# Kernel tuning notes

Hardware: AMD Instinct MI355X
Metric: run time of the kernel (lower is better)

## Reference

```python
import jax, jax.numpy as jnp
import numpy as np

N_RULES = 64  # R
OUT_PER_RULE = 64  # O, fc out = R*O = 4096


def setup_inputs() -> dict:
    key = jax.random.key(0)
    k1, k2, k3, k4 = jax.random.split(key, 4)
    S, D_IN = 8192, 1024
    RO = N_RULES * OUT_PER_RULE
    X = jax.random.normal(k1, (S, D_IN), dtype=jnp.float32)
    # torch.nn.Linear-style weight [out, in] and bias [out]
    W = jax.random.normal(k2, (RO, D_IN), dtype=jnp.float32) * (1.0 / np.sqrt(D_IN))
    b = jax.random.normal(k3, (RO,), dtype=jnp.float32) * 0.01
    # rule firing strengths (computed under no_grad in the original)
    lambdas = jax.random.uniform(k4, (S, N_RULES), dtype=jnp.float32)
    return {"X": X, "W": W, "b": b, "lambdas": lambdas}


def reference(X, W, b, lambdas):
    # fc + sigmoid: [S, R*O]
    H = jax.nn.sigmoid(X @ W.T + b)
    S = H.shape[0]
    # apply_rule_strength: block-diagonal lambda_eye @ H^T is exactly a
    # rule-weighted sum over the R consecutive O-sized blocks of H.
    Hr = H.reshape(S, N_RULES, OUT_PER_RULE)  # [S, R, O]
    Y = jnp.einsum("sr,sro->so", lambdas, Hr)  # [S, O]
    return Y
```

## Files before the change

kernel.cpp:

```cpp
#include <hip/hip_runtime.h>

#define S_DIM 8192
#define K_DIM 1024
#define RO_DIM 4096
#define O_DIM 64
#define SO (S_DIM * O_DIM)

typedef __attribute__((ext_vector_type(8))) __bf16 bf16x8;
typedef __attribute__((ext_vector_type(4))) float floatx4;
typedef __attribute__((ext_vector_type(4))) unsigned short ushx4;

__device__ inline unsigned short f2bf(float f) {
  unsigned u = __builtin_bit_cast(unsigned, f);
  u += 0x7fff + ((u >> 16) & 1);
  return (unsigned short)(u >> 16);
}
__device__ inline float bf2f(unsigned short h) {
  unsigned u = ((unsigned)h) << 16;
  return __builtin_bit_cast(float, u);
}

__global__ __launch_bounds__(256) void cast_kernel(const float* __restrict__ X,
                                                   const float* __restrict__ W,
                                                   unsigned short* __restrict__ Xb,
                                                   unsigned short* __restrict__ Wb) {
  const int NX4 = (S_DIM * K_DIM) / 4;
#pragma unroll
  for (int i = 0; i < 4; ++i) {
    int g = blockIdx.x * 1024 + i * 256 + threadIdx.x;
    float4 v;
    unsigned short* dst;
    if (g < NX4) {
      v = ((const float4*)X)[g];
      dst = Xb + (size_t)g * 4;
    } else {
      int j = g - NX4;
      v = ((const float4*)W)[j];
      dst = Wb + (size_t)j * 4;
    }
    ushx4 o;
    o.x = f2bf(v.x); o.y = f2bf(v.y); o.z = f2bf(v.z); o.w = f2bf(v.w);
    *(ushx4*)dst = o;
  }
}

__global__ __launch_bounds__(256) void gemm_kernel(const unsigned short* __restrict__ Xb,
                                                   const unsigned short* __restrict__ Wb,
                                                   const float* __restrict__ bias,
                                                   const float* __restrict__ lam,
                                                   unsigned short* __restrict__ partial) {
  __shared__ __align__(16) unsigned char smem[33792];
  unsigned short* Atile = (unsigned short*)smem;
  unsigned short* Btile = (unsigned short*)(smem + 16384);
  float* lamsh = (float*)(smem + 32768);

  const int t = threadIdx.x;
  const int lane = t & 63;
  const int w = t >> 6;
  const int wm = w & 1;
  const int oh = w >> 1;
  const int quad = lane >> 4;
  const int l16 = lane & 15;
  const int gm0 = blockIdx.y * 128;
  const int gn0 = blockIdx.x * 128;

  {
    int row = t >> 1, rl = t & 1;
    lamsh[t] = lam[(size_t)(gm0 + row) * 64 + blockIdx.x * 2 + rl];
  }

  floatx4 acc[4][2][2];
#pragma unroll
  for (int rh = 0; rh < 2; ++rh)
#pragma unroll
    for (int ni = 0; ni < 2; ++ni) {
      float bv = bias[gn0 + rh * 64 + oh * 32 + ni * 16 + l16];
#pragma unroll
      for (int mi = 0; mi < 4; ++mi)
        acc[mi][rh][ni] = (floatx4){bv, bv, bv, bv};
    }

  for (int k0 = 0; k0 < K_DIM; k0 += 64) {
    __syncthreads();
#pragma unroll
    for (int i = 0; i < 4; ++i) {
      int idx = i * 256 + t;
      int row = idx >> 3;
      int cc = idx & 7;
      int gcc = cc ^ (row & 7);
      const unsigned short* ga = Xb + (size_t)(gm0 + row) * K_DIM + k0 + gcc * 8;
      const unsigned short* gb = Wb + (size_t)(gn0 + row) * K_DIM + k0 + gcc * 8;
      __builtin_amdgcn_global_load_lds(
          (const __attribute__((address_space(1))) void*)ga,
          (__attribute__((address_space(3))) void*)(Atile + idx * 8), 16, 0, 0);
      __builtin_amdgcn_global_load_lds(
          (const __attribute__((address_space(1))) void*)gb,
          (__attribute__((address_space(3))) void*)(Btile + idx * 8), 16, 0, 0);
    }
    __syncthreads();

#pragma unroll
    for (int s = 0; s < 2; ++s) {
      bf16x8 af[4], bfr[2][2];
#pragma unroll
      for (int mi = 0; mi < 4; ++mi) {
        int row = wm * 64 + mi * 16 + l16;
        int cc = (s * 4 + quad) ^ (row & 7);
        af[mi] = *(const bf16x8*)(Atile + row * 64 + cc * 8);
      }
#pragma unroll
      for (int rh = 0; rh < 2; ++rh)
#pragma unroll
        for (int ni = 0; ni < 2; ++ni) {
          int row = rh * 64 + oh * 32 + ni * 16 + l16;
          int cc = (s * 4 + quad) ^ (row & 7);
          bfr[rh][ni] = *(const bf16x8*)(Btile + row * 64 + cc * 8);
        }
#pragma unroll
      for (int mi = 0; mi < 4; ++mi)
#pragma unroll
        for (int rh = 0; rh < 2; ++rh)
#pragma unroll
          for (int ni = 0; ni < 2; ++ni)
            acc[mi][rh][ni] =
                __builtin_amdgcn_mfma_f32_16x16x32_bf16(af[mi], bfr[rh][ni], acc[mi][rh][ni], 0, 0, 0);
    }
  }

  unsigned short* pbase = partial + (size_t)blockIdx.x * SO + (size_t)gm0 * O_DIM;
#pragma unroll
  for (int mi = 0; mi < 4; ++mi) {
#pragma unroll
    for (int reg = 0; reg < 4; ++reg) {
      int row = wm * 64 + mi * 16 + quad * 4 + reg;
      float2 lv = *(const float2*)(lamsh + row * 2);
#pragma unroll
      for (int ni = 0; ni < 2; ++ni) {
        float h0 = 1.f / (1.f + __expf(-acc[mi][0][ni][reg]));
        float h1 = 1.f / (1.f + __expf(-acc[mi][1][ni][reg]));
        float y = lv.x * h0 + lv.y * h1;
        pbase[(size_t)row * O_DIM + oh * 32 + ni * 16 + l16] = f2bf(y);
      }
    }
  }
}

__global__ __launch_bounds__(256) void reduce_kernel(const unsigned short* __restrict__ partial,
                                                     float* __restrict__ Y) {
  int i4 = blockIdx.x * 256 + threadIdx.x;
  float s0 = 0.f, s1 = 0.f, s2 = 0.f, s3 = 0.f;
#pragma unroll
  for (int c = 0; c < 32; ++c) {
    ushx4 v = ((const ushx4*)(partial + (size_t)c * SO))[i4];
    s0 += bf2f(v.x); s1 += bf2f(v.y); s2 += bf2f(v.z); s3 += bf2f(v.w);
  }
  ((float4*)Y)[i4] = (float4){s0, s1, s2, s3};
}

extern "C" void kernel_launch(void* const* d_in, const int* in_sizes, int n_in,
                              void* d_out, int out_size, void* d_ws, size_t ws_size,
                              hipStream_t stream) {
  const float* X = (const float*)d_in[0];
  const float* W = (const float*)d_in[1];
  const float* b = (const float*)d_in[2];
  const float* lam = (const float*)d_in[3];
  float* Y = (float*)d_out;

  unsigned short* Xb = (unsigned short*)d_ws;
  unsigned short* Wb = Xb + (size_t)S_DIM * K_DIM;
  unsigned short* partial = Wb + (size_t)RO_DIM * K_DIM;

  int nCast = ((S_DIM + RO_DIM) * K_DIM / 4) / 1024;
  cast_kernel<<<nCast, 256, 0, stream>>>(X, W, Xb, Wb);

  dim3 g(RO_DIM / 128, S_DIM / 128);
  gemm_kernel<<<g, 256, 0, stream>>>(Xb, Wb, b, lam, partial);

  reduce_kernel<<<SO / 1024, 256, 0, stream>>>(partial, Y);
}
```

Measured before the change: 186.9 us.

## Accumulate four rule tiles per GEMM block to shrink split-N partials

Each GEMM block now loops over four consecutive 128-column rule tiles and accumulates the lambda-weighted sigmoid outputs in registers, so only 8 partial slices are written instead of 32. The reduce kernel reads 8 slices in a blocked layout rather than 32. This cuts partial write and read traffic, but the grid shrinks from 2048 to 512 blocks, which lowers parallelism on a 256-CU part. It also adds live registers for the extra accumulators.

```diff
diff --git a/kernel.cpp b/kernel.cpp
--- a/kernel.cpp
+++ b/kernel.cpp
@@ -5,6 +5,7 @@
 #define RO_DIM 4096
 #define O_DIM 64
 #define SO (S_DIM * O_DIM)
+#define NSLICE 8
 
 typedef __attribute__((ext_vector_type(8))) __bf16 bf16x8;
 typedef __attribute__((ext_vector_type(4))) float floatx4;
@@ -62,99 +63,124 @@
   const int quad = lane >> 4;
   const int l16 = lane & 15;
   const int gm0 = blockIdx.y * 128;
-  const int gn0 = blockIdx.x * 128;
-
-  {
-    int row = t >> 1, rl = t & 1;
-    lamsh[t] = lam[(size_t)(gm0 + row) * 64 + blockIdx.x * 2 + rl];
+
+  float yacc[4][4][2];
+#pragma unroll
+  for (int mi = 0; mi < 4; ++mi)
+#pragma unroll
+    for (int reg = 0; reg < 4; ++reg) {
+      yacc[mi][reg][0] = 0.f;
+      yacc[mi][reg][1] = 0.f;
+    }
+
+  for (int rt = 0; rt < 4; ++rt) {
+    const int gn0 = blockIdx.x * 512 + rt * 128;
+    __syncthreads();
+    {
+      int row = t >> 1, rl = t & 1;
+      lamsh[t] = lam[(size_t)(gm0 + row) * 64 + blockIdx.x * 8 + rt * 2 + rl];
+    }
+
+    floatx4 acc[4][2][2];
+#pragma unroll
+    for (int rh = 0; rh < 2; ++rh)
+#pragma unroll
+      for (int ni = 0; ni < 2; ++ni) {
+        float bv = bias[gn0 + rh * 64 + oh * 32 + ni * 16 + l16];
+#pragma unroll
+        for (int mi = 0; mi < 4; ++mi)
+          acc[mi][rh][ni] = (floatx4){bv, bv, bv, bv};
+      }
+
+    for (int k0 = 0; k0 < K_DIM; k0 += 64) {
+      __syncthreads();
+#pragma unroll
+      for (int i = 0; i < 4; ++i) {
+        int idx = i * 256 + t;
+        int row = idx >> 3;
+        int cc = idx & 7;
+        int gcc = cc ^ (row & 7);
+        const unsigned short* ga = Xb + (size_t)(gm0 + row) * K_DIM + k0 + gcc * 8;
+        const unsigned short* gb = Wb + (size_t)(gn0 + row) * K_DIM + k0 + gcc * 8;
+        __builtin_amdgcn_global_load_lds(
+            (const __attribute__((address_space(1))) void*)ga,
+            (__attribute__((address_space(3))) void*)(Atile + idx * 8), 16, 0, 0);
+        __builtin_amdgcn_global_load_lds(
+            (const __attribute__((address_space(1))) void*)gb,
+            (__attribute__((address_space(3))) void*)(Btile + idx * 8), 16, 0, 0);
+      }
+      __syncthreads();
+
+#pragma unroll
+      for (int s = 0; s < 2; ++s) {
+        bf16x8 af[4], bfr[2][2];
+#pragma unroll
+        for (int mi = 0; mi < 4; ++mi) {
+          int row = wm * 64 + mi * 16 + l16;
+          int cc = (s * 4 + quad) ^ (row & 7);
+          af[mi] = *(const bf16x8*)(Atile + row * 64 + cc * 8);
+        }
+#pragma unroll
+        for (int rh = 0; rh < 2; ++rh)
+#pragma unroll
+          for (int ni = 0; ni < 2; ++ni) {
+            int row = rh * 64 + oh * 32 + ni * 16 + l16;
+            int cc = (s * 4 + quad) ^ (row & 7);
+            bfr[rh][ni] = *(const bf16x8*)(Btile + row * 64 + cc * 8);
+          }
+#pragma unroll
+        for (int mi = 0; mi < 4; ++mi)
+#pragma unroll
+          for (int rh = 0; rh < 2; ++rh)
+#pragma unroll
+            for (int ni = 0; ni < 2; ++ni)
+              acc[mi][rh][ni] = __builtin_amdgcn_mfma_f32_16x16x32_bf16(
+                  af[mi], bfr[rh][ni], acc[mi][rh][ni], 0, 0, 0);
+      }
+    }
+
+#pragma unroll
+    for (int mi = 0; mi < 4; ++mi) {
+#pragma unroll
+      for (int reg = 0; reg < 4; ++reg) {
+        int row = wm * 64 + mi * 16 + quad * 4 + reg;
+        float2 lv = *(const float2*)(lamsh + row * 2);
+#pragma unroll
+        for (int ni = 0; ni < 2; ++ni) {
+          float h0 = 1.f / (1.f + __expf(-acc[mi][0][ni][reg]));
+          float h1 = 1.f / (1.f + __expf(-acc[mi][1][ni][reg]));
+          yacc[mi][reg][ni] += lv.x * h0 + lv.y * h1;
+        }
+      }
+    }
   }
 
-  floatx4 acc[4][2][2];
-#pragma unroll
-  for (int rh = 0; rh < 2; ++rh)
-#pragma unroll
-    for (int ni = 0; ni < 2; ++ni) {
-      float bv = bias[gn0 + rh * 64 + oh * 32 + ni * 16 + l16];
-#pragma unroll
-      for (int mi = 0; mi < 4; ++mi)
-        acc[mi][rh][ni] = (floatx4){bv, bv, bv, bv};
-    }
-
-  for (int k0 = 0; k0 < K_DIM; k0 += 64) {
-    __syncthreads();
-#pragma unroll
-    for (int i = 0; i < 4; ++i) {
-      int idx = i * 256 + t;
-      int row = idx >> 3;
-      int cc = idx & 7;
-      int gcc = cc ^ (row & 7);
-      const unsigned short* ga = Xb + (size_t)(gm0 + row) * K_DIM + k0 + gcc * 8;
-      const unsigned short* gb = Wb + (size_t)(gn0 + row) * K_DIM + k0 + gcc * 8;
-      __builtin_amdgcn_global_load_lds(
-          (const __attribute__((address_space(1))) void*)ga,
-          (__attribute__((address_space(3))) void*)(Atile + idx * 8), 16, 0, 0);
-      __builtin_amdgcn_global_load_lds(
-          (const __attribute__((address_space(1))) void*)gb,
-          (__attribute__((address_space(3))) void*)(Btile + idx * 8), 16, 0, 0);
-    }
-    __syncthreads();
-
-#pragma unroll
-    for (int s = 0; s < 2; ++s) {
-      bf16x8 af[4], bfr[2][2];
-#pragma unroll
-      for (int mi = 0; mi < 4; ++mi) {
-        int row = wm * 64 + mi * 16 + l16;
-        int cc = (s * 4 + quad) ^ (row & 7);
-        af[mi] = *(const bf16x8*)(Atile + row * 64 + cc * 8);
-      }
-#pragma unroll
-      for (int rh = 0; rh < 2; ++rh)
-#pragma unroll
-        for (int ni = 0; ni < 2; ++ni) {
-          int row = rh * 64 + oh * 32 + ni * 16 + l16;
-          int cc = (s * 4 + quad) ^ (row & 7);
-          bfr[rh][ni] = *(const bf16x8*)(Btile + row * 64 + cc * 8);
-        }
-#pragma unroll
-      for (int mi = 0; mi < 4; ++mi)
-#pragma unroll
-        for (int rh = 0; rh < 2; ++rh)
-#pragma unroll
-          for (int ni = 0; ni < 2; ++ni)
-            acc[mi][rh][ni] =
-                __builtin_amdgcn_mfma_f32_16x16x32_bf16(af[mi], bfr[rh][ni], acc[mi][rh][ni], 0, 0, 0);
-    }
-  }
-
-  unsigned short* pbase = partial + (size_t)blockIdx.x * SO + (size_t)gm0 * O_DIM;
-#pragma unroll
-  for (int mi = 0; mi < 4; ++mi) {
+  unsigned short* pbase = partial + ((size_t)blockIdx.y * NSLICE + blockIdx.x) * (128 * O_DIM);
+#pragma unroll
+  for (int mi = 0; mi < 4; ++mi)
 #pragma unroll
     for (int reg = 0; reg < 4; ++reg) {
       int row = wm * 64 + mi * 16 + quad * 4 + reg;
-      float2 lv = *(const float2*)(lamsh + row * 2);
-#pragma unroll
-      for (int ni = 0; ni < 2; ++ni) {
-        float h0 = 1.f / (1.f + __expf(-acc[mi][0][ni][reg]));
-        float h1 = 1.f / (1.f + __expf(-acc[mi][1][ni][reg]));
-        float y = lv.x * h0 + lv.y * h1;
-        pbase[(size_t)row * O_DIM + oh * 32 + ni * 16 + l16] = f2bf(y);
-      }
-    }
-  }
+#pragma unroll
+      for (int ni = 0; ni < 2; ++ni)
+        pbase[(size_t)row * O_DIM + oh * 32 + ni * 16 + l16] = f2bf(yacc[mi][reg][ni]);
+    }
 }
 
 __global__ __launch_bounds__(256) void reduce_kernel(const unsigned short* __restrict__ partial,
                                                      float* __restrict__ Y) {
-  int i4 = blockIdx.x * 256 + threadIdx.x;
+  int g = blockIdx.x * 256 + threadIdx.x;
+  int e = g * 4;
+  int by = e >> 13;
+  int local = e & 8191;
+  const unsigned short* base = partial + (size_t)by * NSLICE * 8192 + local;
   float s0 = 0.f, s1 = 0.f, s2 = 0.f, s3 = 0.f;
 #pragma unroll
-  for (int c = 0; c < 32; ++c) {
-    ushx4 v = ((const ushx4*)(partial + (size_t)c * SO))[i4];
+  for (int c = 0; c < NSLICE; ++c) {
+    ushx4 v = *(const ushx4*)(base + c * 8192);
     s0 += bf2f(v.x); s1 += bf2f(v.y); s2 += bf2f(v.z); s3 += bf2f(v.w);
   }
-  ((float4*)Y)[i4] = (float4){s0, s1, s2, s3};
+  ((float4*)Y)[g] = (float4){s0, s1, s2, s3};
 }
 
 extern "C" void kernel_launch(void* const* d_in, const int* in_sizes, int n_in,
@@ -173,7 +199,7 @@
   int nCast = ((S_DIM + RO_DIM) * K_DIM / 4) / 1024;
   cast_kernel<<<nCast, 256, 0, stream>>>(X, W, Xb, Wb);
 
-  dim3 g(RO_DIM / 128, S_DIM / 128);
+  dim3 g(RO_DIM / 512, S_DIM / 128);
   gemm_kernel<<<g, 256, 0, stream>>>(Xb, Wb, b, lam, partial);
 
   reduce_kernel<<<SO / 1024, 256, 0, stream>>>(partial, Y);
```

New measurement: 193.0 us. 1.03x slower.

## Pre-swizzle W into MFMA fragment layout and load B directly to registers

Applied to the files above, without the earlier changes.

The cast kernel now writes W in bf16 in a fragment-ordered layout (16-row groups, 8-element k chunks) so each lane can load its MFMA B operand with one contiguous 16-byte global load. The GEMM drops the B LDS tile and its LDS reads, halving shared memory use and possibly raising occupancy. The cost is that B fragments come straight from global/L2 with no LDS reuse across waves, and these loads are issued before the barrier without double buffering, which may expose latency.

```diff
diff --git a/kernel.cpp b/kernel.cpp
--- a/kernel.cpp
+++ b/kernel.cpp
@@ -9,6 +9,7 @@
 typedef __attribute__((ext_vector_type(8))) __bf16 bf16x8;
 typedef __attribute__((ext_vector_type(4))) float floatx4;
 typedef __attribute__((ext_vector_type(4))) unsigned short ushx4;
+typedef __attribute__((ext_vector_type(8))) unsigned short ushx8;
 
 __device__ inline unsigned short f2bf(float f) {
   unsigned u = __builtin_bit_cast(unsigned, f);
@@ -23,36 +24,45 @@
 __global__ __launch_bounds__(256) void cast_kernel(const float* __restrict__ X,
                                                    const float* __restrict__ W,
                                                    unsigned short* __restrict__ Xb,
-                                                   unsigned short* __restrict__ Wb) {
-  const int NX4 = (S_DIM * K_DIM) / 4;
+                                                   unsigned short* __restrict__ Wt) {
+  int b = blockIdx.x;
+  if (b < 2048) {
 #pragma unroll
-  for (int i = 0; i < 4; ++i) {
-    int g = blockIdx.x * 1024 + i * 256 + threadIdx.x;
-    float4 v;
-    unsigned short* dst;
-    if (g < NX4) {
-      v = ((const float4*)X)[g];
-      dst = Xb + (size_t)g * 4;
-    } else {
-      int j = g - NX4;
-      v = ((const float4*)W)[j];
-      dst = Wb + (size_t)j * 4;
+    for (int i = 0; i < 4; ++i) {
+      int g = b * 1024 + i * 256 + threadIdx.x;
+      float4 v = ((const float4*)X)[g];
+      ushx4 o;
+      o.x = f2bf(v.x); o.y = f2bf(v.y); o.z = f2bf(v.z); o.w = f2bf(v.w);
+      *(ushx4*)(Xb + (size_t)g * 4) = o;
     }
-    ushx4 o;
-    o.x = f2bf(v.x); o.y = f2bf(v.y); o.z = f2bf(v.z); o.w = f2bf(v.w);
-    *(ushx4*)dst = o;
+  } else {
+    int wb = b - 2048;
+#pragma unroll
+    for (int i = 0; i < 4; ++i) {
+      int c = wb * 1024 + i * 256 + threadIdx.x;
+      int n16 = c >> 11;
+      int r = c & 2047;
+      int kc = r >> 4;
+      int nl = r & 15;
+      const float* src = W + (size_t)(n16 * 16 + nl) * K_DIM + kc * 8;
+      float4 v0 = *(const float4*)src;
+      float4 v1 = *(const float4*)(src + 4);
+      ushx8 o;
+      o[0] = f2bf(v0.x); o[1] = f2bf(v0.y); o[2] = f2bf(v0.z); o[3] = f2bf(v0.w);
+      o[4] = f2bf(v1.x); o[5] = f2bf(v1.y); o[6] = f2bf(v1.z); o[7] = f2bf(v1.w);
+      *(ushx8*)(Wt + (size_t)c * 8) = o;
+    }
   }
 }
 
 __global__ __launch_bounds__(256) void gemm_kernel(const unsigned short* __restrict__ Xb,
-                                                   const unsigned short* __restrict__ Wb,
+                                                   const unsigned short* __restrict__ Wt,
                                                    const float* __restrict__ bias,
                                                    const float* __restrict__ lam,
                                                    unsigned short* __restrict__ partial) {
-  __shared__ __align__(16) unsigned char smem[33792];
+  __shared__ __align__(16) unsigned char smem[17408];
   unsigned short* Atile = (unsigned short*)smem;
-  unsigned short* Btile = (unsigned short*)(smem + 16384);
-  float* lamsh = (float*)(smem + 32768);
+  float* lamsh = (float*)(smem + 16384);
 
   const int t = threadIdx.x;
   const int lane = t & 63;
@@ -63,6 +73,7 @@
   const int l16 = lane & 15;
   const int gm0 = blockIdx.y * 128;
   const int gn0 = blockIdx.x * 128;
+  const int n16base = blockIdx.x * 8;
 
   {
     int row = t >> 1, rl = t & 1;
@@ -89,19 +100,28 @@
       int cc = idx & 7;
       int gcc = cc ^ (row & 7);
       const unsigned short* ga = Xb + (size_t)(gm0 + row) * K_DIM + k0 + gcc * 8;
-      const unsigned short* gb = Wb + (size_t)(gn0 + row) * K_DIM + k0 + gcc * 8;
       __builtin_amdgcn_global_load_lds(
           (const __attribute__((address_space(1))) void*)ga,
           (__attribute__((address_space(3))) void*)(Atile + idx * 8), 16, 0, 0);
-      __builtin_amdgcn_global_load_lds(
-          (const __attribute__((address_space(1))) void*)gb,
-          (__attribute__((address_space(3))) void*)(Btile + idx * 8), 16, 0, 0);
     }
+
+    bf16x8 bfr[2][2][2];
+#pragma unroll
+    for (int s = 0; s < 2; ++s)
+#pragma unroll
+      for (int rh = 0; rh < 2; ++rh)
+#pragma unroll
+        for (int ni = 0; ni < 2; ++ni) {
+          int n16 = n16base + rh * 4 + oh * 2 + ni;
+          int kc = (k0 >> 3) + s * 4 + quad;
+          bfr[s][rh][ni] = *(const bf16x8*)(Wt + (((size_t)n16 * 128 + kc) * 16 + l16) * 8);
+        }
+
     __syncthreads();
 
 #pragma unroll
     for (int s = 0; s < 2; ++s) {
-      bf16x8 af[4], bfr[2][2];
+      bf16x8 af[4];
 #pragma unroll
       for (int mi = 0; mi < 4; ++mi) {
         int row = wm * 64 + mi * 16 + l16;
@@ -109,21 +129,13 @@
         af[mi] = *(const bf16x8*)(Atile + row * 64 + cc * 8);
       }
 #pragma unroll
-      for (int rh = 0; rh < 2; ++rh)
-#pragma unroll
-        for (int ni = 0; ni < 2; ++ni) {
-          int row = rh * 64 + oh * 32 + ni * 16 + l16;
-          int cc = (s * 4 + quad) ^ (row & 7);
-          bfr[rh][ni] = *(const bf16x8*)(Btile + row * 64 + cc * 8);
-        }
-#pragma unroll
       for (int mi = 0; mi < 4; ++mi)
 #pragma unroll
         for (int rh = 0; rh < 2; ++rh)
 #pragma unroll
           for (int ni = 0; ni < 2; ++ni)
-            acc[mi][rh][ni] =
-                __builtin_amdgcn_mfma_f32_16x16x32_bf16(af[mi], bfr[rh][ni], acc[mi][rh][ni], 0, 0, 0);
+            acc[mi][rh][ni] = __builtin_amdgcn_mfma_f32_16x16x32_bf16(
+                af[mi], bfr[s][rh][ni], acc[mi][rh][ni], 0, 0, 0);
     }
   }
 
@@ -167,14 +179,13 @@
   float* Y = (float*)d_out;
 
   unsigned short* Xb = (unsigned short*)d_ws;
-  unsigned short* Wb = Xb + (size_t)S_DIM * K_DIM;
-  unsigned short* partial = Wb + (size_t)RO_DIM * K_DIM;
+  unsigned short* Wt = Xb + (size_t)S_DIM * K_DIM;
+  unsigned short* partial = Wt + (size_t)RO_DIM * K_DIM;
 
-  int nCast = ((S_DIM + RO_DIM) * K_DIM / 4) / 1024;
-  cast_kernel<<<nCast, 256, 0, stream>>>(X, W, Xb, Wb);
+  cast_kernel<<<2560, 256, 0, stream>>>(X, W, Xb, Wt);
 
   dim3 g(RO_DIM / 128, S_DIM / 128);
-  gemm_kernel<<<g, 256, 0, stream>>>(Xb, Wb, b, lam, partial);
+  gemm_kernel<<<g, 256, 0, stream>>>(Xb, Wt, b, lam, partial);
 
   reduce_kernel<<<SO / 1024, 256, 0, stream>>>(partial, Y);
 }
```

Result: no change. 187.9 us (+0.6%).
